# Performance work log

Hardware: AMD Instinct MI355X
Metric: run time of the kernel (lower is better)

The kernel has to match this reference:

```python
import jax, jax.numpy as jnp
import numpy as np

N = 50000      # nodes
K = 16         # neighbors per node (adj has K+1 cols; col 0 = self, sliced off)
NFEAT = 128
NHID = 128
NCLASS = 64
SLOPE = 0.2    # LeakyReLU slope used by Tail-GNN Relation module


def _relation(xg, mean_x, G1, G2, B1, B2, r):
    # xg: [N,K,F] gathered neighbor features, mean_x: [N,F] weighted mean
    # FiLM-style relation (TransE translation), mean-pooled over neighbors
    nb = (mean_x @ G2)[:, None, :]
    gamma = jax.nn.leaky_relu(jnp.einsum('nkf,fg->nkg', xg, G1) + nb, SLOPE) + 1.0
    nb2 = (mean_x @ B2)[:, None, :]
    beta = jax.nn.leaky_relu(jnp.einsum('nkf,fg->nkg', xg, B1) + nb2, SLOPE)
    r_v = gamma * r + beta                       # [N,K,F]
    return jnp.mean(xg + r_v - mean_x[:, None, :], axis=1)  # [N,F]


def _lrgcn(x, idx, w1, w2, W, G1, G2, B1, B2, r):
    nbr = idx[:, 1:]                              # [N,K] drop self column
    xg = x[nbr]                                   # [N,K,F] irregular gather
    mean_x = jnp.mean(xg * w1[:, 1:, None], axis=1)   # [N,F]
    m = _relation(xg, mean_x, G1, G2, B1, B2, r)      # [N,F]
    # tail=False branch: embed = mean_k(W(xg) * w2); W is linear (no bias)
    # so aggregate first, then transform (same math, less memory)
    embed = jnp.mean(xg * w2[:, 1:, None], axis=1) @ W  # [N,H]
    return embed, m


def setup_inputs() -> dict:
    key = jax.random.key(0)
    ks = jax.random.split(key, 20)
    s = 0.05
    inp = {
        'x': jax.random.normal(ks[0], (N, NFEAT), jnp.float32),
        'adj1_idx': jax.random.randint(ks[1], (N, K + 1), 0, N),
        'adj1_w1': jax.random.uniform(ks[2], (N, K + 1), jnp.float32),
        'adj1_w2': jax.random.uniform(ks[3], (N, K + 1), jnp.float32),
        'adj2_idx': jax.random.randint(ks[4], (N, K + 1), 0, N),
        'adj2_w1': jax.random.uniform(ks[5], (N, K + 1), jnp.float32),
        'adj2_w2': jax.random.uniform(ks[6], (N, K + 1), jnp.float32),
        'W1': jax.random.normal(ks[7], (NFEAT, NHID), jnp.float32) * s,
        'W2': jax.random.normal(ks[8], (NHID, NCLASS), jnp.float32) * s,
        'r1_G1': jax.random.normal(ks[9], (NFEAT, NFEAT), jnp.float32) * s,
        'r1_G2': jax.random.normal(ks[10], (NFEAT, NFEAT), jnp.float32) * s,
        'r1_B1': jax.random.normal(ks[11], (NFEAT, NFEAT), jnp.float32) * s,
        'r1_B2': jax.random.normal(ks[12], (NFEAT, NFEAT), jnp.float32) * s,
        'r1_r': jax.random.normal(ks[13], (NFEAT,), jnp.float32) * s,
        'r2_G1': jax.random.normal(ks[14], (NHID, NHID), jnp.float32) * s,
        'r2_G2': jax.random.normal(ks[15], (NHID, NHID), jnp.float32) * s,
        'r2_B1': jax.random.normal(ks[16], (NHID, NHID), jnp.float32) * s,
        'r2_B2': jax.random.normal(ks[17], (NHID, NHID), jnp.float32) * s,
        'r2_r': jax.random.normal(ks[18], (NHID,), jnp.float32) * s,
    }
    return inp


def reference(x, adj1_idx, adj1_w1, adj1_w2, adj2_idx, adj2_w1, adj2_w2,
              W1, W2, r1_G1, r1_G2, r1_B1, r1_B2, r1_r,
              r2_G1, r2_G2, r2_B1, r2_B2, r2_r):
    h1, m1 = _lrgcn(x, adj1_idx, adj1_w1, adj1_w2, W1,
                    r1_G1, r1_G2, r1_B1, r1_B2, r1_r)
    # eval mode: dropout is identity
    h1 = jax.nn.elu(h1)
    h2, m2 = _lrgcn(h1, adj2_idx, adj2_w1, adj2_w2, W2,
                    r2_G1, r2_G2, r2_B1, r2_B2, r2_r)
    return h2  # [N, NCLASS]
```

## Files before the change

kernel.cpp:

```cpp
#include <hip/hip_runtime.h>
#include <hip/hip_bf16.h>


#define NN   50000
#define KNBR 16
#define NF   128
#define NC   64

typedef short s16x8 __attribute__((ext_vector_type(8)));
typedef float f32x4 __attribute__((ext_vector_type(4)));

static __device__ __forceinline__ unsigned short f2bf(float f) {
  __hip_bfloat16 h = __float2bfloat16(f);
  return reinterpret_cast<unsigned short&>(h);
}
static __device__ __forceinline__ float bflo(unsigned int u) {
  return __uint_as_float(u << 16);
}
static __device__ __forceinline__ float bfhi(unsigned int u) {
  return __uint_as_float(u & 0xffff0000u);
}

__global__ __launch_bounds__(256, 2) void gemm_mfma_128(
    const float* __restrict__ A, const float* __restrict__ B,
    unsigned short* __restrict__ C, int M) {
  constexpr int CT = 8;
  constexpr int KP = 136;
  __shared__ unsigned short Wt_s[128 * KP];
  __shared__ unsigned short st_s[4][16 * KP];

  const int t = threadIdx.x;
  for (int i = t; i < 128 * 128; i += 256) {
    const int k = i >> 7, c = i & 127;
    Wt_s[c * KP + k] = f2bf(B[i]);
  }
  __syncthreads();

  const int w   = t >> 6;
  const int l   = t & 63;
  const int lr  = l & 15;
  const int lk  = l >> 4;
  const int bm0 = blockIdx.x * 128 + w * 32;

  const int row0 = bm0 + lr, row1 = row0 + 16;
  const int r0c = row0 < M ? row0 : M - 1;
  const int r1c = row1 < M ? row1 : M - 1;

  f32x4 acc[2][CT];
#pragma unroll
  for (int mt = 0; mt < 2; ++mt)
#pragma unroll
    for (int ct = 0; ct < CT; ++ct) acc[mt][ct] = (f32x4){0.f, 0.f, 0.f, 0.f};

  const float4* A4 = reinterpret_cast<const float4*>(A);
#pragma unroll
  for (int ks = 0; ks < 4; ++ks) {
    const float4 u0 = A4[(size_t)r0c * 32 + ks * 8 + lk * 2];
    const float4 u1 = A4[(size_t)r0c * 32 + ks * 8 + lk * 2 + 1];
    const float4 v0 = A4[(size_t)r1c * 32 + ks * 8 + lk * 2];
    const float4 v1 = A4[(size_t)r1c * 32 + ks * 8 + lk * 2 + 1];
    unsigned short a0[8] = {f2bf(u0.x), f2bf(u0.y), f2bf(u0.z), f2bf(u0.w),
                            f2bf(u1.x), f2bf(u1.y), f2bf(u1.z), f2bf(u1.w)};
    unsigned short a1[8] = {f2bf(v0.x), f2bf(v0.y), f2bf(v0.z), f2bf(v0.w),
                            f2bf(v1.x), f2bf(v1.y), f2bf(v1.z), f2bf(v1.w)};
    s16x8 af0 = __builtin_bit_cast(s16x8, *(uint4*)a0);
    s16x8 af1 = __builtin_bit_cast(s16x8, *(uint4*)a1);
    const int kb = ks * 32 + lk * 8;
#pragma unroll
    for (int ct = 0; ct < CT; ++ct) {
      const uint4 bw = *reinterpret_cast<const uint4*>(&Wt_s[(ct * 16 + lr) * KP + kb]);
      const s16x8 bf = __builtin_bit_cast(s16x8, bw);
      acc[0][ct] = __builtin_amdgcn_mfma_f32_16x16x32_bf16(af0, bf, acc[0][ct], 0, 0, 0);
      acc[1][ct] = __builtin_amdgcn_mfma_f32_16x16x32_bf16(af1, bf, acc[1][ct], 0, 0, 0);
    }
  }

  unsigned short* st = st_s[w];
#pragma unroll
  for (int mt = 0; mt < 2; ++mt) {
#pragma unroll
    for (int ct = 0; ct < CT; ++ct)
#pragma unroll
      for (int r = 0; r < 4; ++r)
        st[(lk * 4 + r) * KP + ct * 16 + lr] = f2bf(acc[mt][ct][r]);
#pragma unroll
    for (int p = 0; p < 4; ++p) {
      const int ri = p * 4 + lk;
      const int grow = bm0 + mt * 16 + ri;
      if (grow < M) {
        const uint4 v = *reinterpret_cast<const uint4*>(&st[ri * KP + lr * 8]);
        *reinterpret_cast<uint4*>(&C[(size_t)grow * NF + lr * 8]) = v;
      }
    }
  }
}

__global__ __launch_bounds__(512, 4) void gather_gemm_fused(
    const unsigned short* __restrict__ Y1, const int* __restrict__ idx,
    const float* __restrict__ w, const float* __restrict__ W2,
    unsigned short* __restrict__ Y2) {
  constexpr int KP = 136;
  __shared__ int   idx_s[64][KNBR];
  __shared__ float w_s[64][KNBR];
  __shared__ unsigned short Wt_s[64 * KP];
  __shared__ unsigned short h1_s[64 * KP];
  __shared__ unsigned short st_s[8][16 * 40];

  const int t  = threadIdx.x;
  const int n0 = blockIdx.x * 64;

#pragma unroll
  for (int j = 0; j < 2; ++j) {
    const int i = t + j * 512;
    const int node = i >> 4, k = i & 15;
    int gn = n0 + node; if (gn >= NN) gn = NN - 1;
    const int g = gn * (KNBR + 1) + 1 + k;
    idx_s[node][k] = idx[g];
    w_s[node][k]   = w[g];
  }
#pragma unroll
  for (int j = 0; j < 16; ++j) {
    const int i = t + j * 512;
    const int k = i >> 6, c = i & 63;
    Wt_s[c * KP + k] = f2bf(W2[i]);
  }
  __syncthreads();

  const uint4* Y14 = reinterpret_cast<const uint4*>(Y1);
  {
    const int l = t & 15;
#pragma unroll
    for (int half = 0; half < 2; ++half) {
      const int n = half * 32 + (t >> 4);
      uint4 v[KNBR];
#pragma unroll
      for (int k = 0; k < KNBR; ++k)
        v[k] = Y14[(size_t)idx_s[n][k] * 16 + l];
      float acc[8];
#pragma unroll
      for (int j = 0; j < 8; ++j) acc[j] = 0.f;
#pragma unroll
      for (int k = 0; k < KNBR; ++k) {
        const float wv = w_s[n][k];
        acc[0] += wv * bflo(v[k].x); acc[1] += wv * bfhi(v[k].x);
        acc[2] += wv * bflo(v[k].y); acc[3] += wv * bfhi(v[k].y);
        acc[4] += wv * bflo(v[k].z); acc[5] += wv * bfhi(v[k].z);
        acc[6] += wv * bflo(v[k].w); acc[7] += wv * bfhi(v[k].w);
      }
      uint4 r;
      unsigned int* rp = &r.x;
#pragma unroll
      for (int j = 0; j < 4; ++j) {
        float a = acc[2 * j] * (1.f / KNBR);
        float b = acc[2 * j + 1] * (1.f / KNBR);
        a = a > 0.f ? a : expm1f(a);
        b = b > 0.f ? b : expm1f(b);
        rp[j] = (unsigned int)f2bf(a) | ((unsigned int)f2bf(b) << 16);
      }
      *reinterpret_cast<uint4*>(&h1_s[n * KP + l * 8]) = r;
    }
  }
  __syncthreads();

  {
    const int wv_ = t >> 6;
    const int l   = t & 63;
    const int lr  = l & 15;
    const int lk  = l >> 4;
    const int mt  = wv_ >> 1;
    const int ch  = wv_ & 1;

    f32x4 acc[2];
    acc[0] = (f32x4){0.f, 0.f, 0.f, 0.f};
    acc[1] = (f32x4){0.f, 0.f, 0.f, 0.f};
#pragma unroll
    for (int ks = 0; ks < 4; ++ks) {
      const int kb = ks * 32 + lk * 8;
      const uint4 aw = *reinterpret_cast<const uint4*>(&h1_s[(mt * 16 + lr) * KP + kb]);
      const s16x8 af = __builtin_bit_cast(s16x8, aw);
#pragma unroll
      for (int ct = 0; ct < 2; ++ct) {
        const uint4 bw = *reinterpret_cast<const uint4*>(
            &Wt_s[(ch * 32 + ct * 16 + lr) * KP + kb]);
        const s16x8 bf = __builtin_bit_cast(s16x8, bw);
        acc[ct] = __builtin_amdgcn_mfma_f32_16x16x32_bf16(af, bf, acc[ct], 0, 0, 0);
      }
    }

    unsigned short* st = st_s[wv_];
#pragma unroll
    for (int ct = 0; ct < 2; ++ct)
#pragma unroll
      for (int r = 0; r < 4; ++r)
        st[(lk * 4 + r) * 40 + ct * 16 + lr] = f2bf(acc[ct][r]);
    const int ri = l >> 2;
    const int grow = n0 + mt * 16 + ri;
    if (grow < NN) {
      const uint4 v = *reinterpret_cast<const uint4*>(&st[ri * 40 + (l & 3) * 8]);
      *reinterpret_cast<uint4*>(&Y2[(size_t)grow * NC + ch * 32 + (l & 3) * 8]) = v;
    }
  }
}

__global__ __launch_bounds__(512) void gather_mean_out(
    const unsigned short* __restrict__ Y2, const int* __restrict__ idx,
    const float* __restrict__ w, float* __restrict__ out) {
  __shared__ int   idx_s[64][KNBR];
  __shared__ float w_s[64][KNBR];
  const int t  = threadIdx.x;
  const int n0 = blockIdx.x * 64;
#pragma unroll
  for (int j = 0; j < 2; ++j) {
    const int i = t + j * 512;
    const int node = i >> 4, k = i & 15;
    int gn = n0 + node; if (gn >= NN) gn = NN - 1;
    const int g = gn * (KNBR + 1) + 1 + k;
    idx_s[node][k] = idx[g];
    w_s[node][k]   = w[g];
  }
  __syncthreads();

  const int n = t >> 3, l = t & 7;
  const int gn = n0 + n;
  if (gn >= NN) return;
  const uint4* Y24 = reinterpret_cast<const uint4*>(Y2);
  uint4 v[KNBR];
#pragma unroll
  for (int k = 0; k < KNBR; ++k)
    v[k] = Y24[(size_t)idx_s[n][k] * 8 + l];
  float acc[8];
#pragma unroll
  for (int j = 0; j < 8; ++j) acc[j] = 0.f;
#pragma unroll
  for (int k = 0; k < KNBR; ++k) {
    const float wv = w_s[n][k];
    acc[0] += wv * bflo(v[k].x); acc[1] += wv * bfhi(v[k].x);
    acc[2] += wv * bflo(v[k].y); acc[3] += wv * bfhi(v[k].y);
    acc[4] += wv * bflo(v[k].z); acc[5] += wv * bfhi(v[k].z);
    acc[6] += wv * bflo(v[k].w); acc[7] += wv * bfhi(v[k].w);
  }
  float4* o4 = reinterpret_cast<float4*>(out);
  const size_t ob = ((size_t)gn * NC + l * 8) >> 2;
  o4[ob] = make_float4(acc[0] * (1.f / KNBR), acc[1] * (1.f / KNBR),
                       acc[2] * (1.f / KNBR), acc[3] * (1.f / KNBR));
  o4[ob + 1] = make_float4(acc[4] * (1.f / KNBR), acc[5] * (1.f / KNBR),
                           acc[6] * (1.f / KNBR), acc[7] * (1.f / KNBR));
}

extern "C" void kernel_launch(void* const* d_in, const int* in_sizes, int n_in,
                              void* d_out, int out_size, void* d_ws,
                              size_t ws_size, hipStream_t stream) {
  const float* x   = (const float*)d_in[0];
  const int*   a1i = (const int*)d_in[1];
  const float* a1w = (const float*)d_in[3];
  const int*   a2i = (const int*)d_in[4];
  const float* a2w = (const float*)d_in[6];
  const float* W1  = (const float*)d_in[7];
  const float* W2  = (const float*)d_in[8];
  float*       out = (float*)d_out;

  unsigned short* Y1 = (unsigned short*)d_ws;
  unsigned short* Y2 = Y1 + (size_t)NN * NF;

  gemm_mfma_128<<<(NN + 127) / 128, 256, 0, stream>>>(x, W1, Y1, NN);
  gather_gemm_fused<<<(NN + 63) / 64, 512, 0, stream>>>(Y1, a1i, a1w, W2, Y2);
  gather_mean_out<<<(NN + 63) / 64, 512, 0, stream>>>(Y2, a2i, a2w, out);
}
```

Before: 58.67 us.

## Partition neighbor gathers into index-range passes with block barriers for cache locality

Both gather kernels now split neighbor reads into passes by source-node index range (4 ranges for Y1, 2 for Y2), with a block-wide barrier after each pass. The aim is to keep concurrently running blocks working on the same slice of the feature table, so L2/MALL hit rates go up on the random gathers. Index and weight loads switch to nontemporal loads, and the output kernel gains an occupancy hint. The cost is extra barriers, predicated loads and less memory-level parallelism per pass. Blocks are also not synchronized across the GPU, so the intended locality is not guaranteed.

```diff
diff --git a/kernel.cpp b/kernel.cpp
--- a/kernel.cpp
+++ b/kernel.cpp
@@ -115,8 +115,8 @@
     const int node = i >> 4, k = i & 15;
     int gn = n0 + node; if (gn >= NN) gn = NN - 1;
     const int g = gn * (KNBR + 1) + 1 + k;
-    idx_s[node][k] = idx[g];
-    w_s[node][k]   = w[g];
+    idx_s[node][k] = __builtin_nontemporal_load(&idx[g]);
+    w_s[node][k]   = __builtin_nontemporal_load(&w[g]);
   }
 #pragma unroll
   for (int j = 0; j < 16; ++j) {
@@ -128,31 +128,68 @@
 
   const uint4* Y14 = reinterpret_cast<const uint4*>(Y1);
   {
-    const int l = t & 15;
+    const int l  = t & 15;
+    const int na = t >> 4;
+    const int nb = 32 + na;
+    float accA[8], accB[8];
+#pragma unroll
+    for (int j = 0; j < 8; ++j) { accA[j] = 0.f; accB[j] = 0.f; }
+
+    for (int pass = 0; pass < 4; ++pass) {
+      const unsigned lo = (unsigned)(pass * 12500);
+      uint4 v[KNBR];
+      unsigned mk;
+      mk = 0;
+#pragma unroll
+      for (int k = 0; k < KNBR; ++k) {
+        const unsigned id = (unsigned)idx_s[na][k];
+        if (id - lo < 12500u) {
+          v[k] = Y14[(size_t)id * 16 + l];
+          mk |= 1u << k;
+        }
+      }
+#pragma unroll
+      for (int k = 0; k < KNBR; ++k) {
+        if (mk & (1u << k)) {
+          const float wv = w_s[na][k];
+          accA[0] += wv * bflo(v[k].x); accA[1] += wv * bfhi(v[k].x);
+          accA[2] += wv * bflo(v[k].y); accA[3] += wv * bfhi(v[k].y);
+          accA[4] += wv * bflo(v[k].z); accA[5] += wv * bfhi(v[k].z);
+          accA[6] += wv * bflo(v[k].w); accA[7] += wv * bfhi(v[k].w);
+        }
+      }
+      mk = 0;
+#pragma unroll
+      for (int k = 0; k < KNBR; ++k) {
+        const unsigned id = (unsigned)idx_s[nb][k];
+        if (id - lo < 12500u) {
+          v[k] = Y14[(size_t)id * 16 + l];
+          mk |= 1u << k;
+        }
+      }
+#pragma unroll
+      for (int k = 0; k < KNBR; ++k) {
+        if (mk & (1u << k)) {
+          const float wv = w_s[nb][k];
+          accB[0] += wv * bflo(v[k].x); accB[1] += wv * bfhi(v[k].x);
+          accB[2] += wv * bflo(v[k].y); accB[3] += wv * bfhi(v[k].y);
+          accB[4] += wv * bflo(v[k].z); accB[5] += wv * bfhi(v[k].z);
+          accB[6] += wv * bflo(v[k].w); accB[7] += wv * bfhi(v[k].w);
+        }
+      }
+      __syncthreads();
+    }
+
 #pragma unroll
     for (int half = 0; half < 2; ++half) {
-      const int n = half * 32 + (t >> 4);
-      uint4 v[KNBR];
-#pragma unroll
-      for (int k = 0; k < KNBR; ++k)
-        v[k] = Y14[(size_t)idx_s[n][k] * 16 + l];
-      float acc[8];
-#pragma unroll
-      for (int j = 0; j < 8; ++j) acc[j] = 0.f;
-#pragma unroll
-      for (int k = 0; k < KNBR; ++k) {
-        const float wv = w_s[n][k];
-        acc[0] += wv * bflo(v[k].x); acc[1] += wv * bfhi(v[k].x);
-        acc[2] += wv * bflo(v[k].y); acc[3] += wv * bfhi(v[k].y);
-        acc[4] += wv * bflo(v[k].z); acc[5] += wv * bfhi(v[k].z);
-        acc[6] += wv * bflo(v[k].w); acc[7] += wv * bfhi(v[k].w);
-      }
+      const float* ac = half ? accB : accA;
+      const int    n  = half ? nb : na;
       uint4 r;
       unsigned int* rp = &r.x;
 #pragma unroll
       for (int j = 0; j < 4; ++j) {
-        float a = acc[2 * j] * (1.f / KNBR);
-        float b = acc[2 * j + 1] * (1.f / KNBR);
+        float a = ac[2 * j] * (1.f / KNBR);
+        float b = ac[2 * j + 1] * (1.f / KNBR);
         a = a > 0.f ? a : expm1f(a);
         b = b > 0.f ? b : expm1f(b);
         rp[j] = (unsigned int)f2bf(a) | ((unsigned int)f2bf(b) << 16);
@@ -202,7 +239,7 @@
   }
 }
 
-__global__ __launch_bounds__(512) void gather_mean_out(
+__global__ __launch_bounds__(512, 4) void gather_mean_out(
     const unsigned short* __restrict__ Y2, const int* __restrict__ idx,
     const float* __restrict__ w, float* __restrict__ out) {
   __shared__ int   idx_s[64][KNBR];
@@ -215,36 +252,52 @@
     const int node = i >> 4, k = i & 15;
     int gn = n0 + node; if (gn >= NN) gn = NN - 1;
     const int g = gn * (KNBR + 1) + 1 + k;
-    idx_s[node][k] = idx[g];
-    w_s[node][k]   = w[g];
+    idx_s[node][k] = __builtin_nontemporal_load(&idx[g]);
+    w_s[node][k]   = __builtin_nontemporal_load(&w[g]);
   }
   __syncthreads();
 
   const int n = t >> 3, l = t & 7;
   const int gn = n0 + n;
-  if (gn >= NN) return;
+  const bool valid = gn < NN;
   const uint4* Y24 = reinterpret_cast<const uint4*>(Y2);
-  uint4 v[KNBR];
-#pragma unroll
-  for (int k = 0; k < KNBR; ++k)
-    v[k] = Y24[(size_t)idx_s[n][k] * 8 + l];
   float acc[8];
 #pragma unroll
   for (int j = 0; j < 8; ++j) acc[j] = 0.f;
-#pragma unroll
-  for (int k = 0; k < KNBR; ++k) {
-    const float wv = w_s[n][k];
-    acc[0] += wv * bflo(v[k].x); acc[1] += wv * bfhi(v[k].x);
-    acc[2] += wv * bflo(v[k].y); acc[3] += wv * bfhi(v[k].y);
-    acc[4] += wv * bflo(v[k].z); acc[5] += wv * bfhi(v[k].z);
-    acc[6] += wv * bflo(v[k].w); acc[7] += wv * bfhi(v[k].w);
-  }
-  float4* o4 = reinterpret_cast<float4*>(out);
-  const size_t ob = ((size_t)gn * NC + l * 8) >> 2;
-  o4[ob] = make_float4(acc[0] * (1.f / KNBR), acc[1] * (1.f / KNBR),
-                       acc[2] * (1.f / KNBR), acc[3] * (1.f / KNBR));
-  o4[ob + 1] = make_float4(acc[4] * (1.f / KNBR), acc[5] * (1.f / KNBR),
-                           acc[6] * (1.f / KNBR), acc[7] * (1.f / KNBR));
+
+  for (int pass = 0; pass < 2; ++pass) {
+    const unsigned lo = (unsigned)(pass * 25000);
+    uint4 v[KNBR];
+    unsigned mk = 0;
+#pragma unroll
+    for (int k = 0; k < KNBR; ++k) {
+      const unsigned id = (unsigned)idx_s[n][k];
+      if (id - lo < 25000u) {
+        v[k] = Y24[(size_t)id * 8 + l];
+        mk |= 1u << k;
+      }
+    }
+#pragma unroll
+    for (int k = 0; k < KNBR; ++k) {
+      if (mk & (1u << k)) {
+        const float wv = w_s[n][k];
+        acc[0] += wv * bflo(v[k].x); acc[1] += wv * bfhi(v[k].x);
+        acc[2] += wv * bflo(v[k].y); acc[3] += wv * bfhi(v[k].y);
+        acc[4] += wv * bflo(v[k].z); acc[5] += wv * bfhi(v[k].z);
+        acc[6] += wv * bflo(v[k].w); acc[7] += wv * bfhi(v[k].w);
+      }
+    }
+    __syncthreads();
+  }
+
+  if (valid) {
+    float4* o4 = reinterpret_cast<float4*>(out);
+    const size_t ob = ((size_t)gn * NC + l * 8) >> 2;
+    o4[ob] = make_float4(acc[0] * (1.f / KNBR), acc[1] * (1.f / KNBR),
+                         acc[2] * (1.f / KNBR), acc[3] * (1.f / KNBR));
+    o4[ob + 1] = make_float4(acc[4] * (1.f / KNBR), acc[5] * (1.f / KNBR),
+                             acc[6] * (1.f / KNBR), acc[7] * (1.f / KNBR));
+  }
 }
 
 extern "C" void kernel_launch(void* const* d_in, const int* in_sizes, int n_in,
```

Result: slower. 120.0 us (+104.5%).
